# Optimization experiments

Hardware: AMD Instinct MI355X
Metric: run time of the kernel (lower is better)

The kernel has to match this reference:

```python
import jax, jax.numpy as jnp
import numpy as np

SCALE, R_MAX, ALPHA = 16, 8, 2.0
HL, WL, C_FEAT = 16, 16, 384
HH, WH = HL * SCALE, WL * SCALE


def bilinear_resize(img, out_h, out_w):
    """PyTorch F.interpolate(mode='bilinear', align_corners=False, antialias=False).
    img: [..., H, W] -> [..., out_h, out_w]."""
    H, W = img.shape[-2], img.shape[-1]
    ys = jnp.maximum((jnp.arange(out_h, dtype=jnp.float32) + 0.5) * (H / out_h) - 0.5, 0.0)
    xs = jnp.maximum((jnp.arange(out_w, dtype=jnp.float32) + 0.5) * (W / out_w) - 0.5, 0.0)
    y0 = jnp.floor(ys).astype(jnp.int32)
    x0 = jnp.floor(xs).astype(jnp.int32)
    y1 = jnp.minimum(y0 + 1, H - 1)
    x1 = jnp.minimum(x0 + 1, W - 1)
    wy = (ys - y0)[:, None]
    wx = (xs - x0)[None, :]
    g = lambda yi, xi: img[..., yi[:, None], xi[None, :]]
    return ((1 - wy) * (1 - wx) * g(y0, x0) + (1 - wy) * wx * g(y0, x1)
            + wy * (1 - wx) * g(y1, x0) + wy * wx * g(y1, x1))


def jbu_forward(feat_lr, guide_hr, sx_raw, sy_raw, th_raw, sr_raw):
    C, Hl, Wl = feat_lr.shape[1], feat_lr.shape[2], feat_lr.shape[3]
    Hh, Wh = guide_hr.shape[2], guide_hr.shape[3]
    scale, R_max, alpha = SCALE, R_MAX, ALPHA
    NEG = -1e30  # finite stand-in for -inf (keeps grads NaN-free)

    # parameter transforms from the module
    sx = jnp.exp(sx_raw[0, 0])
    sy = jnp.exp(sy_raw[0, 0])
    th = jnp.pi * jnp.tanh(th_raw[0, 0])
    sr = jnp.exp(sr_raw[0, 0])

    Y, X = jnp.meshgrid(jnp.arange(Hh, dtype=jnp.float32),
                        jnp.arange(Wh, dtype=jnp.float32), indexing='ij')
    u = (Y + 0.5) / scale - 0.5
    v = (X + 0.5) / scale - 0.5
    uc = jnp.clip(jnp.round(u), 0, Hl - 1).astype(jnp.int32)
    vc = jnp.clip(jnp.round(v), 0, Wl - 1).astype(jnp.int32)

    sigma_eff_hr = bilinear_resize(jnp.maximum(sx, sy), Hh, Wh)
    R_map = jnp.clip(jnp.ceil(alpha * sigma_eff_hr), 1.0, float(R_max))  # [Hh,Wh]

    offs = jnp.arange(-R_max, R_max + 1, dtype=jnp.int32)
    dYg, dXg = jnp.meshgrid(offs, offs, indexing='ij')
    dY = dYg.reshape(-1)[:, None, None]  # [N,1,1]
    dX = dXg.reshape(-1)[:, None, None]

    Ui = jnp.clip(uc[None] + dY, 0, Hl - 1)  # [N,Hh,Wh]
    Vi = jnp.clip(vc[None] + dX, 0, Wl - 1)
    idx = Ui * Wl + Vi                       # flat LR index per (neighbor, HR pixel)
    gat = lambda mp: mp.reshape(-1)[idx]

    sxg = jnp.maximum(gat(sx), 1e-6)
    syg = jnp.maximum(gat(sy), 1e-6)
    thg = gat(th)
    srg = jnp.maximum(gat(sr), 1e-6)

    dx = X[None] - ((Vi.astype(jnp.float32) + 0.5) * scale - 0.5)
    dyv = Y[None] - ((Ui.astype(jnp.float32) + 0.5) * scale - 0.5)
    ct, st = jnp.cos(thg), jnp.sin(thg)
    a = dx * ct + dyv * st
    b = -dx * st + dyv * ct

    guide_lr = bilinear_resize(guide_hr[0], Hl, Wl)  # [3,Hl,Wl]
    g_diff2 = sum((guide_hr[0, c][None] - gat(guide_lr[c])) ** 2 for c in range(3))

    log_w = (-a * a / (2 * sxg ** 2 + 1e-8)
             - b * b / (2 * syg ** 2 + 1e-8)
             - g_diff2 / (2.0 * srg ** 2 + 1e-8))  # [N,Hh,Wh]

    mask = (dY * dY + dX * dX).astype(jnp.float32) <= R_map[None] ** 2
    log_w = jnp.where(mask, log_w, NEG)

    # numerically stable softmax over neighbors (== online-softmax result)
    m = log_w.max(axis=0)
    s = jnp.exp(log_w - m[None])  # masked entries underflow to 0
    den = s.sum(axis=0)           # [Hh,Wh]

    # num[c,h,w] = sum_n s[n,h,w] * feat[idx[n,h,w], c]
    # scatter neighbor weights by LR pixel, then one GEMM with the LR features
    N = idx.shape[0]
    idx2 = idx.reshape(N, Hh * Wh)
    cols = jnp.arange(Hh * Wh, dtype=jnp.int32)[None, :]
    acc = jnp.zeros((Hl * Wl, Hh * Wh), jnp.float32).at[idx2, cols].add(s.reshape(N, -1))
    feat_flat = feat_lr[0].reshape(C, Hl * Wl)  # [C, P]
    num = jnp.einsum('cp,pq->cq', feat_flat, acc).reshape(C, Hh, Wh)

    return (num / jnp.maximum(den, 1e-8)[None])[None]  # [1,C,Hh,Wh]


def setup_inputs() -> dict:
    key = jax.random.key(0)
    k1, k2, k3, k4, k5, k6 = jax.random.split(key, 6)
    feat_lr = jax.random.normal(k1, (1, C_FEAT, HL, WL), jnp.float32)
    guide_hr = jax.random.uniform(k2, (1, 3, HH, WH), dtype=jnp.float32)
    log_sigma = float(np.log(16.0))
    log_sigma_r = float(np.log(0.12))
    sx_raw = log_sigma + 0.1 * jax.random.normal(k3, (1, 1, HL, WL), jnp.float32)
    sy_raw = log_sigma + 0.1 * jax.random.normal(k4, (1, 1, HL, WL), jnp.float32)
    th_raw = 0.1 * jax.random.normal(k5, (1, 1, HL, WL), jnp.float32)
    sr_raw = log_sigma_r + 0.1 * jax.random.normal(k6, (1, 1, HL, WL), jnp.float32)
    return {"feat_lr": feat_lr, "guide_hr": guide_hr, "sx_raw": sx_raw,
            "sy_raw": sy_raw, "th_raw": th_raw, "sr_raw": sr_raw}


def reference(feat_lr, guide_hr, sx_raw, sy_raw, th_raw, sr_raw):
    return jbu_forward(feat_lr, guide_hr, sx_raw, sy_raw, th_raw, sr_raw)
```

## Files before the change

kernel.cpp:

```cpp
#include <hip/hip_runtime.h>
#include <math.h>

#define NEG_BIG  (-1e30f)
#define NEG_H16  (-60000.0f)

typedef _Float16 half8  __attribute__((ext_vector_type(8)));
typedef _Float16 half2v __attribute__((ext_vector_type(2)));
typedef float    floatx4 __attribute__((ext_vector_type(4)));

__global__ __launch_bounds__(256) void setup_all(
    const float* __restrict__ feat, const float* __restrict__ guide,
    const float* __restrict__ sx_raw, const float* __restrict__ sy_raw,
    const float* __restrict__ th_raw, const float* __restrict__ sr_raw,
    _Float16* __restrict__ feat16, float4* __restrict__ PA,
    float4* __restrict__ PB, float* __restrict__ PS,
    _Float16* __restrict__ LCtab)
{
    const int b = blockIdx.x, t = threadIdx.x;
    if (b < 48) {
        int i = (b*256 + t)*8;
        float4 f0 = *(const float4*)(feat + i);
        float4 f1 = *(const float4*)(feat + i + 4);
        half8 h;
        h[0]=(_Float16)f0.x; h[1]=(_Float16)f0.y; h[2]=(_Float16)f0.z; h[3]=(_Float16)f0.w;
        h[4]=(_Float16)f1.x; h[5]=(_Float16)f1.y; h[6]=(_Float16)f1.z; h[7]=(_Float16)f1.w;
        *(half8*)(feat16 + i) = h;
        return;
    }
    if (b == 48) {
        float sx = expf(sx_raw[t]);
        float sy = expf(sy_raw[t]);
        float th = 3.14159265358979323846f * tanhf(th_raw[t]);
        float sr = expf(sr_raw[t]);
        float sxg = fmaxf(sx, 1e-6f), syg = fmaxf(sy, 1e-6f), srg = fmaxf(sr, 1e-6f);
        float iA = 1.f / (2.f*sxg*sxg + 1e-8f);
        float iB = 1.f / (2.f*syg*syg + 1e-8f);
        float iC = 1.f / (2.f*srg*srg + 1e-8f);
        float ct = cosf(th), st = sinf(th);
        float A2 = iA*ct*ct + iB*st*st;
        float B2 = 2.f*ct*st*(iA - iB);
        float C2 = iA*st*st + iB*ct*ct;
        PA[t] = make_float4(-A2, -B2, -C2, -iC);
        int i = t >> 4, j = t & 15;
        int y0 = 16*i + 7, x0 = 16*j + 7;
        float g[3];
#pragma unroll
        for (int c = 0; c < 3; ++c) {
            const float* gp = guide + c*65536;
            g[c] = 0.25f*(gp[y0*256 + x0]     + gp[y0*256 + x0 + 1] +
                          gp[(y0+1)*256 + x0] + gp[(y0+1)*256 + x0 + 1]);
        }
        PB[t] = make_float4(2.f*iC*g[0], 2.f*iC*g[1], 2.f*iC*g[2],
                            -iC*(g[0]*g[0] + g[1]*g[1] + g[2]*g[2]));
        PS[t] = fmaxf(sx, sy);
        return;
    }
    const int tb  = b - 49;
    const int uc  = tb >> 3;
    const int vc0 = (tb & 7) << 1;
    const int Pu  = t >> 4;
    const int col = t & 15;
    const int Rt  = (col >> 1) + 1;
    const int vc  = vc0 + (col & 1);
    const int R2  = Rt * Rt;
    int ylo = (Pu == 0)  ? -8 : (Pu - uc);
    int yhi = (Pu == 15) ?  8 : (Pu - uc);
    ylo = max(ylo, -8); yhi = min(yhi, 8);
    int cnt[16];
#pragma unroll
    for (int Pv = 1; Pv < 15; ++Pv) {
        int d = Pv - vc;
        int lim = R2 - d*d;
        int c = 0;
        if (lim >= 0 && ylo <= yhi) {
            int s = (int)sqrtf((float)lim);
            c = max(0, min(yhi, s) - max(ylo, -s) + 1);
        }
        cnt[Pv] = c;
    }
    cnt[0] = 0;
    if (-vc >= -8) {
        for (int dY = ylo; dY <= yhi; ++dY) {
            int lim = R2 - dY*dY;
            if (lim >= 0) {
                int r = (int)sqrtf((float)lim);
                cnt[0] += max(0, min(-vc, r) + r + 1);
            }
        }
    }
    cnt[15] = 0;
    if (15 - vc <= 8) {
        for (int dY = ylo; dY <= yhi; ++dY) {
            int lim = R2 - dY*dY;
            if (lim >= 0) {
                int r = (int)sqrtf((float)lim);
                cnt[15] += max(0, r - max(15 - vc, -r) + 1);
            }
        }
    }
    _Float16* dst = LCtab + (size_t)tb * 4096;
#pragma unroll
    for (int Pv = 0; Pv < 16; ++Pv)
        dst[(Pu*16 + Pv)*16 + col] = (_Float16)
            ((cnt[Pv] > 0) ? __logf((float)cnt[Pv]) : NEG_H16);
}

__global__ __launch_bounds__(512) void jbu_main(
    const float* __restrict__ guide, const _Float16* __restrict__ feat16,
    const float4* __restrict__ PA, const float4* __restrict__ PB,
    const float* __restrict__ PS, const _Float16* __restrict__ LCtab,
    float* __restrict__ out)
{
    __shared__ __align__(16) _Float16 Wb[32][256];
    __shared__ float4 sPA[256];
    __shared__ float4 sPB[256];
    __shared__ __align__(16) _Float16 LCh[4096];
    __shared__ float redM[8][32];
    __shared__ float redD[8][32];

    const int t   = threadIdx.x;
    const int q   = t & 31;
    const int grp = t >> 5;
    const int wv  = t >> 6;
    const int Y   = blockIdx.y;
    const int X0  = blockIdx.x << 5;
    const int X   = X0 + q;
    const float Yf = (float)Y, Xf = (float)X;
    const int uc   = Y >> 4;

    if (t < 256) sPA[t] = PA[t];
    else         sPB[t & 255] = PB[t & 255];
    {
        const float4* Lsrc =
            (const float4*)(LCtab + (size_t)(uc*8 + blockIdx.x) * 4096);
        ((float4*)LCh)[t] = Lsrc[t];
    }

    float u = (Yf + 0.5f)*0.0625f - 0.5f;
    float v = (Xf + 0.5f)*0.0625f - 0.5f;
    float ysc = fmaxf(u, 0.f), xsc = fmaxf(v, 0.f);
    int y0 = (int)ysc, x0 = (int)xsc;
    int y1 = min(y0 + 1, 15), x1 = min(x0 + 1, 15);
    float wy = ysc - (float)y0, wx = xsc - (float)x0;
    float s00 = PS[y0*16 + x0], s01 = PS[y0*16 + x1];
    float s10 = PS[y1*16 + x0], s11 = PS[y1*16 + x1];
    float sig = (1.f - wy)*((1.f - wx)*s00 + wx*s01)
              +        wy *((1.f - wx)*s10 + wx*s11);
    float Rf = fminf(fmaxf(ceilf(2.f*sig), 1.f), 8.f);
    const int colq = ((int)Rf - 1)*2 + (q >> 4);

    const float g0 = guide[          (Y << 8) + X];
    const float g1 = guide[ 65536 + ((Y << 8) + X)];
    const float g2 = guide[131072 + ((Y << 8) + X)];
    const float g2s = g0*g0 + g1*g1 + g2*g2;

    __syncthreads();

    const int pbase = grp << 4;
    const float dy  = Yf - (16.f*(float)grp + 7.5f);
    const float dy2 = dy*dy;
    float lw[16];
    float mloc = NEG_BIG;
#pragma unroll
    for (int col = 0; col < 16; ++col) {
        int p = pbase + col;
        float dx = Xf - (16.f*(float)col + 7.5f);
        float4 A = sPA[p];
        float4 B = sPB[p];
        float w = fmaf(B.x, g0, B.w);
        w = fmaf(B.y, g1, w);
        w = fmaf(B.z, g2, w);
        w = fmaf(A.w, g2s, w);
        w = fmaf(A.x, dx*dx, w);
        w = fmaf(A.y, dx*dy, w);
        w = fmaf(A.z, dy2, w);
        w += (float)LCh[p*16 + colq];
        lw[col] = w;
        mloc = fmaxf(mloc, w);
    }
    mloc = fmaxf(mloc, __shfl_xor(mloc, 32, 64));
    redM[wv][q] = mloc;
    __syncthreads();
    const float m = fmaxf(fmaxf(fmaxf(redM[0][q], redM[1][q]),
                                fmaxf(redM[2][q], redM[3][q])),
                          fmaxf(fmaxf(redM[4][q], redM[5][q]),
                                fmaxf(redM[6][q], redM[7][q])));

    float dloc = 0.f;
#pragma unroll
    for (int col = 0; col < 16; col += 2) {
        int p0 = pbase + col;
        float e0 = __expf(lw[col]     - m);
        float e1 = __expf(lw[col + 1] - m);
        half2v hh; hh[0] = (_Float16)e0; hh[1] = (_Float16)e1;
        int chunk = ((p0 >> 3) ^ q) & 31;
        *(half2v*)&Wb[q][chunk*8 + (p0 & 7)] = hh;
        dloc += (float)hh[0] + (float)hh[1];
    }
    dloc += __shfl_xor(dloc, 32, 64);
    redD[wv][q] = dloc;
    __syncthreads();

    const int lane = t & 63;
    const int mrow = lane & 15;
    const int quad = lane >> 4;
    const int c0   = wv * 48;

    float idv[2];
#pragma unroll
    for (int nt = 0; nt < 2; ++nt) {
        int pix = nt*16 + mrow;
        float den = ((redD[0][pix] + redD[1][pix]) + (redD[2][pix] + redD[3][pix]))
                  + ((redD[4][pix] + redD[5][pix]) + (redD[6][pix] + redD[7][pix]));
        idv[nt] = 1.f / fmaxf(den, 1e-8f);
    }

    floatx4 acc[3][2] = {};
    const _Float16* fbase = feat16 + (c0 + mrow)*256 + quad*8;

#pragma unroll
    for (int ks = 0; ks < 8; ++ks) {
        half8 a[3];
#pragma unroll
        for (int mt = 0; mt < 3; ++mt)
            a[mt] = *(const half8*)(fbase + mt*16*256 + ks*32);
        half8 b[2];
#pragma unroll
        for (int nt = 0; nt < 2; ++nt) {
            int pix = nt*16 + mrow;
            int chunk = ((ks*4 + quad) ^ pix) & 31;
            b[nt] = *(const half8*)(&Wb[pix][chunk*8]);
        }
#pragma unroll
        for (int mt = 0; mt < 3; ++mt)
#pragma unroll
            for (int nt = 0; nt < 2; ++nt)
                acc[mt][nt] = __builtin_amdgcn_mfma_f32_16x16x32_f16(
                    a[mt], b[nt], acc[mt][nt], 0, 0, 0);
    }

    __syncthreads();

    float* Sf = (float*)Wb + (wv << 9);
    const int sch = lane >> 3;
    const int spg = lane & 7;
    const int outcol = (Y << 8) + X0;
#pragma unroll
    for (int mt = 0; mt < 3; ++mt) {
#pragma unroll
        for (int nt = 0; nt < 2; ++nt)
#pragma unroll
            for (int r = 0; r < 4; ++r)
                Sf[(quad*4 + r)*32 + nt*16 + mrow] = acc[mt][nt][r] * idv[nt];
#pragma unroll
        for (int j = 0; j < 2; ++j) {
            float4 vv = *(const float4*)&Sf[(j*8 + sch)*32 + spg*4];
            *(float4*)(out + (size_t)(c0 + mt*16 + j*8 + sch)*65536
                           + outcol + spg*4) = vv;
        }
    }
}

extern "C" void kernel_launch(void* const* d_in, const int* in_sizes, int n_in,
                              void* d_out, int out_size, void* d_ws, size_t ws_size,
                              hipStream_t stream)
{
    const float* feat   = (const float*)d_in[0];
    const float* guide  = (const float*)d_in[1];
    const float* sx_raw = (const float*)d_in[2];
    const float* sy_raw = (const float*)d_in[3];
    const float* th_raw = (const float*)d_in[4];
    const float* sr_raw = (const float*)d_in[5];
    float* out = (float*)d_out;

    char* ws = (char*)d_ws;
    _Float16* feat16 = (_Float16*)ws;
    float4*   PA     = (float4*)(ws + 196608);
    float4*   PB     = (float4*)(ws + 200704);
    float*    PS     = (float*)(ws + 204800);
    _Float16* LCtab  = (_Float16*)(ws + 205824);

    setup_all<<<177, 256, 0, stream>>>(feat, guide, sx_raw, sy_raw, th_raw,
                                       sr_raw, feat16, PA, PB, PS, LCtab);
    jbu_main<<<dim3(8, 256), 512, 0, stream>>>(guide, feat16, PA, PB, PS,
                                               LCtab, out);
}
```

Measured before the change: 161.8 us.

## Widen jbu_main blocks to 64 pixels with 1024 threads and XCD-aware mapping

Each block now handles 64 output pixels per row using 16 wavefronts, one wave per low-res row group. Each wave's neighbour row index is made wave-uniform via readfirstlane, so PA/PB and the log-count table are read straight from global memory instead of being staged in LDS. The log-count table is rebuilt with 4 column centres per tile to match the 64-pixel tile. Blocks are remapped so each XCD works on a contiguous band of rows for better L2 locality. This trades fewer, larger blocks and more LDS per block for less staging and sync work, with some risk of lower occupancy.

After: 164.4 us. No clear change (+1.6%).

```diff
diff --git a/kernel.cpp b/kernel.cpp
--- a/kernel.cpp
+++ b/kernel.cpp
@@ -56,85 +56,82 @@
         return;
     }
     const int tb  = b - 49;
-    const int uc  = tb >> 3;
-    const int vc0 = (tb & 7) << 1;
+    const int uc  = tb >> 2;
+    const int vc0 = (tb & 3) << 2;
     const int Pu  = t >> 4;
-    const int col = t & 15;
-    const int Rt  = (col >> 1) + 1;
-    const int vc  = vc0 + (col & 1);
-    const int R2  = Rt * Rt;
+    const int colb = t & 15;
     int ylo = (Pu == 0)  ? -8 : (Pu - uc);
     int yhi = (Pu == 15) ?  8 : (Pu - uc);
     ylo = max(ylo, -8); yhi = min(yhi, 8);
-    int cnt[16];
-#pragma unroll
-    for (int Pv = 1; Pv < 15; ++Pv) {
-        int d = Pv - vc;
-        int lim = R2 - d*d;
-        int c = 0;
-        if (lim >= 0 && ylo <= yhi) {
-            int s = (int)sqrtf((float)lim);
-            c = max(0, min(yhi, s) - max(ylo, -s) + 1);
-        }
-        cnt[Pv] = c;
-    }
-    cnt[0] = 0;
-    if (-vc >= -8) {
-        for (int dY = ylo; dY <= yhi; ++dY) {
-            int lim = R2 - dY*dY;
-            if (lim >= 0) {
-                int r = (int)sqrtf((float)lim);
-                cnt[0] += max(0, min(-vc, r) + r + 1);
+    _Float16* dst = LCtab + (size_t)tb * 8192;
+#pragma unroll
+    for (int h = 0; h < 2; ++h) {
+        const int col32 = colb + h*16;
+        const int Rt = (col32 >> 2) + 1;
+        const int vc = vc0 + (col32 & 3);
+        const int R2 = Rt * Rt;
+        int cnt[16];
+#pragma unroll
+        for (int Pv = 1; Pv < 15; ++Pv) {
+            int d = Pv - vc;
+            int lim = R2 - d*d;
+            int c = 0;
+            if (lim >= 0 && ylo <= yhi) {
+                int s = (int)sqrtf((float)lim);
+                c = max(0, min(yhi, s) - max(ylo, -s) + 1);
             }
-        }
-    }
-    cnt[15] = 0;
-    if (15 - vc <= 8) {
-        for (int dY = ylo; dY <= yhi; ++dY) {
-            int lim = R2 - dY*dY;
-            if (lim >= 0) {
-                int r = (int)sqrtf((float)lim);
-                cnt[15] += max(0, r - max(15 - vc, -r) + 1);
+            cnt[Pv] = c;
+        }
+        cnt[0] = 0;
+        if (-vc >= -8) {
+            for (int dY = ylo; dY <= yhi; ++dY) {
+                int lim = R2 - dY*dY;
+                if (lim >= 0) {
+                    int r = (int)sqrtf((float)lim);
+                    cnt[0] += max(0, min(-vc, r) + r + 1);
+                }
             }
         }
-    }
-    _Float16* dst = LCtab + (size_t)tb * 4096;
-#pragma unroll
-    for (int Pv = 0; Pv < 16; ++Pv)
-        dst[(Pu*16 + Pv)*16 + col] = (_Float16)
-            ((cnt[Pv] > 0) ? __logf((float)cnt[Pv]) : NEG_H16);
+        cnt[15] = 0;
+        if (15 - vc <= 8) {
+            for (int dY = ylo; dY <= yhi; ++dY) {
+                int lim = R2 - dY*dY;
+                if (lim >= 0) {
+                    int r = (int)sqrtf((float)lim);
+                    cnt[15] += max(0, r - max(15 - vc, -r) + 1);
+                }
+            }
+        }
+#pragma unroll
+        for (int Pv = 0; Pv < 16; ++Pv)
+            dst[(Pu*16 + Pv)*32 + col32] = (_Float16)
+                ((cnt[Pv] > 0) ? __logf((float)cnt[Pv]) : NEG_H16);
+    }
 }
 
-__global__ __launch_bounds__(512) void jbu_main(
+__global__ __launch_bounds__(1024, 8) void jbu_main(
     const float* __restrict__ guide, const _Float16* __restrict__ feat16,
     const float4* __restrict__ PA, const float4* __restrict__ PB,
     const float* __restrict__ PS, const _Float16* __restrict__ LCtab,
     float* __restrict__ out)
 {
-    __shared__ __align__(16) _Float16 Wb[32][256];
-    __shared__ float4 sPA[256];
-    __shared__ float4 sPB[256];
-    __shared__ __align__(16) _Float16 LCh[4096];
-    __shared__ float redM[8][32];
-    __shared__ float redD[8][32];
-
-    const int t   = threadIdx.x;
-    const int q   = t & 31;
-    const int grp = t >> 5;
-    const int wv  = t >> 6;
-    const int Y   = blockIdx.y;
-    const int X0  = blockIdx.x << 5;
+    __shared__ __align__(16) _Float16 Wb[64][256];
+    __shared__ float redM[16][64];
+    __shared__ float redD[16][64];
+
+    const int t  = threadIdx.x;
+    const int q  = t & 63;
+    const int wv = t >> 6;
+    const int grpu = __builtin_amdgcn_readfirstlane(wv);
+
+    const int n   = blockIdx.x;
+    const int xcd = n & 7;
+    const int s   = n >> 3;
+    const int Y   = xcd*32 + (s >> 2);
+    const int X0  = (s & 3) << 6;
     const int X   = X0 + q;
     const float Yf = (float)Y, Xf = (float)X;
     const int uc   = Y >> 4;
-
-    if (t < 256) sPA[t] = PA[t];
-    else         sPB[t & 255] = PB[t & 255];
-    {
-        const float4* Lsrc =
-            (const float4*)(LCtab + (size_t)(uc*8 + blockIdx.x) * 4096);
-        ((float4*)LCh)[t] = Lsrc[t];
-    }
 
     float u = (Yf + 0.5f)*0.0625f - 0.5f;
     float v = (Xf + 0.5f)*0.0625f - 0.5f;
@@ -147,17 +144,17 @@
     float sig = (1.f - wy)*((1.f - wx)*s00 + wx*s01)
               +        wy *((1.f - wx)*s10 + wx*s11);
     float Rf = fminf(fmaxf(ceilf(2.f*sig), 1.f), 8.f);
-    const int colq = ((int)Rf - 1)*2 + (q >> 4);
+    const int colq = ((int)Rf - 1)*4 + (q >> 4);
 
     const float g0 = guide[          (Y << 8) + X];
     const float g1 = guide[ 65536 + ((Y << 8) + X)];
     const float g2 = guide[131072 + ((Y << 8) + X)];
     const float g2s = g0*g0 + g1*g1 + g2*g2;
 
-    __syncthreads();
-
-    const int pbase = grp << 4;
-    const float dy  = Yf - (16.f*(float)grp + 7.5f);
+    const _Float16* Lb = LCtab + (size_t)(uc*4 + (X0 >> 6))*8192 + colq;
+
+    const int pbase = grpu << 4;
+    const float dy  = Yf - (16.f*(float)grpu + 7.5f);
     const float dy2 = dy*dy;
     float lw[16];
     float mloc = NEG_BIG;
@@ -165,8 +162,8 @@
     for (int col = 0; col < 16; ++col) {
         int p = pbase + col;
         float dx = Xf - (16.f*(float)col + 7.5f);
-        float4 A = sPA[p];
-        float4 B = sPB[p];
+        float4 A = PA[p];
+        float4 B = PB[p];
         float w = fmaf(B.x, g0, B.w);
         w = fmaf(B.y, g1, w);
         w = fmaf(B.z, g2, w);
@@ -174,17 +171,15 @@
         w = fmaf(A.x, dx*dx, w);
         w = fmaf(A.y, dx*dy, w);
         w = fmaf(A.z, dy2, w);
-        w += (float)LCh[p*16 + colq];
+        w += (float)Lb[p*32];
         lw[col] = w;
         mloc = fmaxf(mloc, w);
     }
-    mloc = fmaxf(mloc, __shfl_xor(mloc, 32, 64));
     redM[wv][q] = mloc;
     __syncthreads();
-    const float m = fmaxf(fmaxf(fmaxf(redM[0][q], redM[1][q]),
-                                fmaxf(redM[2][q], redM[3][q])),
-                          fmaxf(fmaxf(redM[4][q], redM[5][q]),
-                                fmaxf(redM[6][q], redM[7][q])));
+    float m = redM[0][q];
+#pragma unroll
+    for (int k = 1; k < 16; ++k) m = fmaxf(m, redM[k][q]);
 
     float dloc = 0.f;
 #pragma unroll
@@ -197,21 +192,24 @@
         *(half2v*)&Wb[q][chunk*8 + (p0 & 7)] = hh;
         dloc += (float)hh[0] + (float)hh[1];
     }
-    dloc += __shfl_xor(dloc, 32, 64);
     redD[wv][q] = dloc;
     __syncthreads();
 
     const int lane = t & 63;
     const int mrow = lane & 15;
     const int quad = lane >> 4;
-    const int c0   = wv * 48;
+    const int cg   = grpu >> 1;
+    const int ph   = grpu & 1;
+    const int c0   = cg * 48;
+    const int pixbase = ph * 32;
 
     float idv[2];
 #pragma unroll
     for (int nt = 0; nt < 2; ++nt) {
-        int pix = nt*16 + mrow;
-        float den = ((redD[0][pix] + redD[1][pix]) + (redD[2][pix] + redD[3][pix]))
-                  + ((redD[4][pix] + redD[5][pix]) + (redD[6][pix] + redD[7][pix]));
+        int pix = pixbase + nt*16 + mrow;
+        float den = 0.f;
+#pragma unroll
+        for (int k = 0; k < 16; ++k) den += redD[k][pix];
         idv[nt] = 1.f / fmaxf(den, 1e-8f);
     }
 
@@ -227,7 +225,7 @@
         half8 b[2];
 #pragma unroll
         for (int nt = 0; nt < 2; ++nt) {
-            int pix = nt*16 + mrow;
+            int pix = pixbase + nt*16 + mrow;
             int chunk = ((ks*4 + quad) ^ pix) & 31;
             b[nt] = *(const half8*)(&Wb[pix][chunk*8]);
         }
@@ -241,10 +239,10 @@
 
     __syncthreads();
 
-    float* Sf = (float*)Wb + (wv << 9);
+    float* Sf = (float*)Wb + (grpu << 9);
     const int sch = lane >> 3;
     const int spg = lane & 7;
-    const int outcol = (Y << 8) + X0;
+    const int outcol = (Y << 8) + X0 + pixbase;
 #pragma unroll
     for (int mt = 0; mt < 3; ++mt) {
 #pragma unroll
@@ -280,8 +278,7 @@
     float*    PS     = (float*)(ws + 204800);
     _Float16* LCtab  = (_Float16*)(ws + 205824);
 
-    setup_all<<<177, 256, 0, stream>>>(feat, guide, sx_raw, sy_raw, th_raw,
+    setup_all<<<113, 256, 0, stream>>>(feat, guide, sx_raw, sy_raw, th_raw,
                                        sr_raw, feat16, PA, PB, PS, LCtab);
-    jbu_main<<<dim3(8, 256), 512, 0, stream>>>(guide, feat16, PA, PB, PS,
-                                               LCtab, out);
+    jbu_main<<<1024, 1024, 0, stream>>>(guide, feat16, PA, PB, PS, LCtab, out);
 }
```
